# Kernel optimization log

Measured on AMD Instinct MI355X. Metric: run time of the kernel, lower is better.

The kernel has to match this reference:

```python
import jax, jax.numpy as jnp
import numpy as np

EPS = 1e-15  # 0.1 ** 15 in the original


def _mi_table(T):
    # Mutual information of a joint-probability table T [nx, ny]
    P_x = jnp.sum(T, axis=1)  # [nx]
    P_y = jnp.sum(T, axis=0)  # [ny]
    T_xy = P_x[:, None] * P_y[None, :]  # outer product [nx, ny]
    mi = jnp.sum(T * (jnp.log((T + EPS) / (T_xy + EPS)) / jnp.log(jnp.float32(2.0))))
    return mi


def setup_inputs() -> dict:
    key = jax.random.key(0)
    k1, k2 = jax.random.split(key)
    N_ins, N_att, K = 16384, 8192, 64
    Ur = jax.random.uniform(k1, (N_ins, K), dtype=jnp.float32)
    Uc = jax.random.uniform(k2, (N_att, K), dtype=jnp.float32)
    return {"Ur": Ur, "Uc": Uc, "nclu_row": K, "nclu_col": K}


def reference(Ur, Uc, nclu_row, nclu_col):
    # joint probability table  [N_ins, N_att]
    T = Ur @ Uc.T
    T = T / jnp.sum(T)

    v1 = jnp.argmax(Ur, axis=1)  # hard row-cluster ids  [N_ins]
    v2 = jnp.argmax(Uc, axis=1)  # hard col-cluster ids  [N_att]

    # Reduce_Table: segment-sum rows then columns (replaces looped mask+concat)
    T_r = jax.ops.segment_sum(T, v1, num_segments=nclu_row)          # [nclu_row, N_att]
    T_rr = jax.ops.segment_sum(T_r.T, v2, num_segments=nclu_col).T  # [nclu_row, nclu_col]

    mi_org = _mi_table(T)
    mi_red = _mi_table(T_rr)

    loss = jnp.log(1.0 + jnp.abs(1.0 - mi_red / mi_org))
    return loss
```

## Files before the change

### kernel.cpp

```cpp
#include <hip/hip_runtime.h>
#include <hip/hip_bf16.h>

#define N_INS 16384
#define N_ATT 8192
#define KDIM  64

typedef __attribute__((ext_vector_type(8))) short bf16x8;
typedef __attribute__((ext_vector_type(4))) float f32x4;

#define OFF_UCB    0
#define OFF_CPR    1048576
#define OFF_CPC    1064960
#define OFF_ASEG   1073152
#define OFF_BSEG   1089536
#define OFF_GACC   1105920
#define OFF_TK     1106688

#define NBLK_SEG   96
#define NBLK_U     96
#define NBLK_HEAVY 2048
#define NBLK_K2    (NBLK_SEG + NBLK_U + NBLK_HEAVY)

__device__ __forceinline__ unsigned short f2bf(float x) {
    unsigned u = __float_as_uint(x);
    u = (u + 0x7FFFu + ((u >> 16) & 1u)) >> 16;
    return (unsigned short)u;
}

__device__ __forceinline__ float wave_red(float v) {
#pragma unroll
    for (int o = 32; o > 0; o >>= 1) v += __shfl_down(v, o, 64);
    return v;
}

typedef __attribute__((address_space(3))) unsigned int as3_u32;
typedef const __attribute__((address_space(1))) unsigned int as1_u32;
__device__ __forceinline__ void stage16(void* l, const void* g) {
    __builtin_amdgcn_global_load_lds((as1_u32*)g, (as3_u32*)l, 16, 0, 0);
}

__global__ __launch_bounds__(256)
void k_prep(const float* __restrict__ Ur, const float* __restrict__ Uc,
            float* __restrict__ cpr, float* __restrict__ cpc,
            unsigned short* __restrict__ Ucb,
            float* __restrict__ Aseg, float* __restrict__ Bseg,
            double* __restrict__ Gacc, unsigned* __restrict__ tickets) {
    __shared__ float cs2[256];
    int blk = blockIdx.x, tid = threadIdx.x;
    if (blk < 128) {
        int gid = blk * 256 + tid;
        for (int c = gid; c < N_ATT * 8; c += 32768) {
            int t = c >> 7, o = c & 127;
            int q, m;
            if (o < 64) { q = o >> 4; m = o & 15; }
            else        { q = 4 + ((o - 64) >> 4); m = (o - 64) & 15; }
            int r = t * 16 + m;
            const float4* src = (const float4*)(Uc + (size_t)r * 64 + q * 8);
            float4 x0 = src[0], x1 = src[1];
            uint4 v;
            v.x = (unsigned)f2bf(x0.x) | ((unsigned)f2bf(x0.y) << 16);
            v.y = (unsigned)f2bf(x0.z) | ((unsigned)f2bf(x0.w) << 16);
            v.z = (unsigned)f2bf(x1.x) | ((unsigned)f2bf(x1.y) << 16);
            v.w = (unsigned)f2bf(x1.z) | ((unsigned)f2bf(x1.w) << 16);
            *(uint4*)((unsigned char*)Ucb + (size_t)c * 16) = v;
        }
        return;
    }
    if (blk == 224) {
        float4 z4 = {0.f, 0.f, 0.f, 0.f};
        for (int i = tid; i < 1024; i += 256) ((float4*)Aseg)[i] = z4;
        for (int i = tid; i < 1024; i += 256) ((float4*)Bseg)[i] = z4;
        if (tid < 96) Gacc[tid] = 0.0;
        if (tid < 64) { tickets[tid] = 0u; tickets[64 + tid] = 0u;
                        tickets[128 + tid] = 0u; tickets[192 + tid] = 0u; }
        if (tid < 16) tickets[256 + tid] = 0u;
        return;
    }
    bool isUr = blk < 192;
    int b = isUr ? (blk - 128) : (blk - 192);
    const float* base = (isUr ? Ur : Uc) + (size_t)b * 256 * KDIM;
    float* dst = (isUr ? cpr : cpc) + b * 64;
    int col = tid & 63, r0 = tid >> 6;
    float s = 0.f;
    for (int r = r0; r < 256; r += 4) s += base[r * KDIM + col];
    cs2[tid] = s;
    __syncthreads();
    if (tid < 64) dst[tid] = cs2[tid] + cs2[tid + 64] + cs2[tid + 128] + cs2[tid + 192];
}

__global__ __launch_bounds__(256)
void k_main(const float* __restrict__ Ur, const float* __restrict__ Uc,
            const unsigned char* __restrict__ Ucb,
            const float* __restrict__ cpr, const float* __restrict__ cpc,
            float* __restrict__ Aseg, float* __restrict__ Bseg,
            double* __restrict__ Gacc, unsigned* __restrict__ tickets,
            float* __restrict__ out) {
    __shared__ __align__(16) unsigned char smem[17408];
    __shared__ int flagS;
    int tid = threadIdx.x, blk = blockIdx.x;
    int wvi = tid >> 6, lane = tid & 63;

    if (blk < NBLK_SEG) {
        float* Part = (float*)smem;
        int*   bins = (int*)(smem + 16384);
        bool isUr = blk < 64;
        int b = isUr ? blk : (blk - 64);
        const float* M = isUr ? Ur : Uc;
        float* Seg = isUr ? Aseg : Bseg;
        int base_row = b * 256;
        for (int i = tid; i < 4096; i += 256) Part[i] = 0.f;
        __syncthreads();
        {
            const float* rp = M + (size_t)(base_row + tid) * KDIM;
            float best = -1e30f; int bidx = 0;
#pragma unroll
            for (int k = 0; k < 64; k += 4) {
                float4 v = *(const float4*)(rp + k);
                if (v.x > best) { best = v.x; bidx = k; }
                if (v.y > best) { best = v.y; bidx = k + 1; }
                if (v.z > best) { best = v.z; bidx = k + 2; }
                if (v.w > best) { best = v.w; bidx = k + 3; }
            }
            bins[tid] = bidx;
        }
        __syncthreads();
        {
            int r0 = wvi * 64;
            const float* Mb = M + (size_t)(base_row + r0) * 64 + lane;
#pragma unroll 4
            for (int r = 0; r < 64; ++r) {
                int bb = bins[r0 + r];
                float val = Mb[(size_t)r * 64];
                atomicAdd(&Part[bb * 64 + lane], val);
            }
        }
        __syncthreads();
        for (int i = tid; i < 4096; i += 256)
            atomicAdd(&Seg[i], Part[i]);
    } else if (blk < NBLK_SEG + NBLK_U) {
        float* wv = (float*)smem;
        bool isUr = blk < (NBLK_SEG + 64);
        int b = isUr ? (blk - NBLK_SEG) : (blk - NBLK_SEG - 64);
        const float* M = isUr ? Ur : Uc;
        int base_row = b * 256;
        if (tid < 64) {
            const float* cpw = isUr ? cpc : cpr;
            int nbw = isUr ? 32 : 64;
            float s = 0.f;
            for (int p = 0; p < nbw; ++p) s += cpw[p * 64 + tid];
            wv[tid] = s;
        }
        __syncthreads();
        const float* rp = M + (size_t)(base_row + tid) * KDIM;
        float u = 0.f;
#pragma unroll
        for (int k = 0; k < 64; k += 4) {
            float4 v = *(const float4*)(rp + k);
            u += v.x * wv[k] + v.y * wv[k + 1] + v.z * wv[k + 2] + v.w * wv[k + 3];
        }
        float pw = wave_red(u * __log2f(u));
        if (lane == 0)
            atomicAdd(&Gacc[(isUr ? 64 : 80) + (b & 15)], (double)pw);
    } else {
        unsigned char* bufs = smem;
        float* gshW = (float*)(smem + 16384);
        int hb = blk - NBLK_SEG - NBLK_U;
        int quad = lane >> 4, m = lane & 15;
        int rb = hb & 127, cc = hb >> 7;
        int row0 = rb * 128 + wvi * 32;
        bf16x8 a[2][2];
#pragma unroll
        for (int t = 0; t < 2; ++t) {
            int ridx = row0 + t * 16 + m;
            const float* rp = Ur + (size_t)ridx * 64 + quad * 8;
#pragma unroll
            for (int h = 0; h < 2; ++h) {
                const float* rph = rp + h * 32;
                float4 x0 = *(const float4*)rph;
                float4 x1 = *(const float4*)(rph + 4);
                bf16x8 f;
                f[0] = (short)f2bf(x0.x); f[1] = (short)f2bf(x0.y);
                f[2] = (short)f2bf(x0.z); f[3] = (short)f2bf(x0.w);
                f[4] = (short)f2bf(x1.x); f[5] = (short)f2bf(x1.y);
                f[6] = (short)f2bf(x1.z); f[7] = (short)f2bf(x1.w);
                a[t][h] = f;
            }
        }
        const unsigned char* gB = Ucb + (size_t)(cc * 32) * 2048;
        int soff = wvi * 2048 + lane * 16;
        stage16(bufs + soff, gB + soff);
        stage16(bufs + soff + 1024, gB + soff + 1024);
        int loff = lane * 16;
        float g = 0.f;
#pragma unroll 1
        for (int pg = 0; pg < 8; ++pg) {
            __syncthreads();
            if (pg < 7) {
                const unsigned char* gn = gB + (size_t)(pg + 1) * 8192;
                unsigned char* bn = bufs + (((pg + 1) & 1) << 13);
                stage16(bn + soff, gn + soff);
                stage16(bn + soff + 1024, gn + soff + 1024);
            }
            const unsigned char* bg = bufs + ((pg & 1) << 13);
#pragma unroll
            for (int p = 0; p < 2; ++p) {
                const unsigned char* bb = bg + p * 4096;
                bf16x8 c00 = *(const bf16x8*)(bb + loff);
                bf16x8 c01 = *(const bf16x8*)(bb + 1024 + loff);
                bf16x8 c10 = *(const bf16x8*)(bb + 2048 + loff);
                bf16x8 c11 = *(const bf16x8*)(bb + 3072 + loff);
                f32x4 acc00 = {0.f,0.f,0.f,0.f}, acc01 = {0.f,0.f,0.f,0.f};
                f32x4 acc10 = {0.f,0.f,0.f,0.f}, acc11 = {0.f,0.f,0.f,0.f};
                acc00 = __builtin_amdgcn_mfma_f32_16x16x32_bf16(a[0][0], c00, acc00, 0, 0, 0);
                acc00 = __builtin_amdgcn_mfma_f32_16x16x32_bf16(a[0][1], c01, acc00, 0, 0, 0);
                acc10 = __builtin_amdgcn_mfma_f32_16x16x32_bf16(a[1][0], c00, acc10, 0, 0, 0);
                acc10 = __builtin_amdgcn_mfma_f32_16x16x32_bf16(a[1][1], c01, acc10, 0, 0, 0);
                acc01 = __builtin_amdgcn_mfma_f32_16x16x32_bf16(a[0][0], c10, acc01, 0, 0, 0);
                acc01 = __builtin_amdgcn_mfma_f32_16x16x32_bf16(a[0][1], c11, acc01, 0, 0, 0);
                acc11 = __builtin_amdgcn_mfma_f32_16x16x32_bf16(a[1][0], c10, acc11, 0, 0, 0);
                acc11 = __builtin_amdgcn_mfma_f32_16x16x32_bf16(a[1][1], c11, acc11, 0, 0, 0);
#pragma unroll
                for (int e = 0; e < 4; ++e) {
                    float d0 = acc00[e]; g += d0 * __log2f(d0);
                    float d1 = acc01[e]; g += d1 * __log2f(d1);
                    float d2 = acc10[e]; g += d2 * __log2f(d2);
                    float d3 = acc11[e]; g += d3 * __log2f(d3);
                }
            }
        }
        float gw = wave_red(g);
        if (lane == 0) gshW[wvi] = gw;
        __syncthreads();
        if (tid == 0) {
            float gs = gshW[0] + gshW[1] + gshW[2] + gshW[3];
            atomicAdd(&Gacc[hb & 63], (double)gs);
        }
    }

    __builtin_amdgcn_s_waitcnt(0);
    __syncthreads();
    if (tid == 0) {
        flagS = 0;
        unsigned old = atomicAdd(&tickets[(blk & 15) << 4], 1u);
        if (old == (NBLK_K2 / 16) - 1) {
            unsigned old2 = atomicAdd(&tickets[256], 1u);
            flagS = (old2 == 15u);
        }
    }
    __syncthreads();
    if (!flagS) return;

    float*  Prx = (float*)smem;
    float*  Pry = (float*)(smem + 256);
    double* sc  = (double*)(smem + 512);
    double* red = (double*)(smem + 1024);
    if (tid < 64) {
        double sa = 0.0, sb = 0.0;
        for (int p = 0; p < 64; ++p) sa += (double)cpr[p * 64 + tid];
        for (int p = 0; p < 32; ++p) sb += (double)cpc[p * 64 + tid];
        red[tid] = sa * sb;
        Prx[tid] = 0.f; Pry[tid] = 0.f;
    }
    __syncthreads();
    if (tid == 0) {
        double s = 0.0;
        for (int k = 0; k < 64; ++k) s += red[k];
        sc[0] = s;
        double gg = 0.0;
        for (int k = 0; k < 64; ++k) gg += Gacc[k];
        sc[1] = gg;
    } else if (tid == 1) {
        double s = 0.0;
        for (int k = 64; k < 80; ++k) s += Gacc[k];
        sc[2] = s;
    } else if (tid == 2) {
        double s = 0.0;
        for (int k = 80; k < 96; ++k) s += Gacc[k];
        sc[3] = s;
    }
    __syncthreads();
    double S = sc[0];
    int p = tid >> 2, q0 = (tid & 3) * 16;
    float tloc[16];
    {
        float prow_sum = 0.f;
        for (int qi = 0; qi < 16; ++qi) {
            int q = q0 + qi;
            double s = 0.0;
            for (int k = 0; k < 64; ++k)
                s += (double)Aseg[p * 64 + k] * (double)Bseg[q * 64 + k];
            float t = (float)(s / S);
            tloc[qi] = t;
            prow_sum += t;
            atomicAdd(&Pry[q], t);
        }
        atomicAdd(&Prx[p], prow_sum);
    }
    __syncthreads();
    {
        const double EPSd = 1e-15;
        double part = 0.0;
        for (int qi = 0; qi < 16; ++qi) {
            double t = (double)tloc[qi];
            double txy = (double)Prx[p] * (double)Pry[q0 + qi];
            part += t * log((t + EPSd) / (txy + EPSd));
        }
        red[tid] = part;
    }
    __syncthreads();
    for (int s2 = 128; s2 > 0; s2 >>= 1) {
        if (tid < s2) red[tid] += red[tid + s2];
        __syncthreads();
    }
    if (tid == 0) {
        const double inv_ln2 = 1.4426950408889634;
        double mi_red = red[0] * inv_ln2;
        double G = sc[1], Uu = sc[2], Vv = sc[3];
        double log2S = log(S) * inv_ln2;
        double mi_org = G / S + log2S - (Uu + Vv) / S;
        double loss = log(1.0 + fabs(1.0 - mi_red / mi_org));
        out[0] = (float)loss;
    }
}

extern "C" void kernel_launch(void* const* d_in, const int* in_sizes, int n_in,
                              void* d_out, int out_size, void* d_ws, size_t ws_size,
                              hipStream_t stream) {
    const float* Ur = (const float*)d_in[0];
    const float* Uc = (const float*)d_in[1];
    float* out = (float*)d_out;
    char* ws = (char*)d_ws;
    unsigned short* Ucb = (unsigned short*)(ws + OFF_UCB);
    float* cpr   = (float*)(ws + OFF_CPR);
    float* cpc   = (float*)(ws + OFF_CPC);
    float* Aseg  = (float*)(ws + OFF_ASEG);
    float* Bseg  = (float*)(ws + OFF_BSEG);
    double* Gacc = (double*)(ws + OFF_GACC);
    unsigned* tickets = (unsigned*)(ws + OFF_TK);

    k_prep<<<225, 256, 0, stream>>>(Ur, Uc, cpr, cpc, Ucb, Aseg, Bseg, Gacc, tickets);
    k_main<<<NBLK_K2, 256, 0, stream>>>(Ur, Uc, (const unsigned char*)Ucb,
                                        cpr, cpc, Aseg, Bseg, Gacc, tickets, out);
}
```

Measured before the change: 161.7 us.

## Read Uc bf16 tiles directly from global and consolidate segment-sum blocks

The heavy MFMA blocks no longer stage Uc bf16 tiles into LDS with double-buffered global_load_lds plus block barriers. They now read the fragments straight from global memory, relying on cache, with the loop unrolled by two. The segment-sum phase uses 16 larger blocks that process 2048 or 1024 rows each. Each block splits the 64 bins into two passes, storing bins as bytes, which shrinks the shared footprint so more blocks fit per CU. The trade is repeated global and L2 traffic and more serial work in fewer seg blocks, in exchange for fewer barriers and fewer global atomics.

```diff
diff --git a/kernel.cpp b/kernel.cpp
--- a/kernel.cpp
+++ b/kernel.cpp
@@ -16,7 +16,7 @@
 #define OFF_GACC   1105920
 #define OFF_TK     1106688
 
-#define NBLK_SEG   96
+#define NBLK_SEG   16
 #define NBLK_U     96
 #define NBLK_HEAVY 2048
 #define NBLK_K2    (NBLK_SEG + NBLK_U + NBLK_HEAVY)
@@ -31,12 +31,6 @@
 #pragma unroll
     for (int o = 32; o > 0; o >>= 1) v += __shfl_down(v, o, 64);
     return v;
-}
-
-typedef __attribute__((address_space(3))) unsigned int as3_u32;
-typedef const __attribute__((address_space(1))) unsigned int as1_u32;
-__device__ __forceinline__ void stage16(void* l, const void* g) {
-    __builtin_amdgcn_global_load_lds((as1_u32*)g, (as3_u32*)l, 16, 0, 0);
 }
 
 __global__ __launch_bounds__(256)
@@ -95,23 +89,21 @@
             float* __restrict__ Aseg, float* __restrict__ Bseg,
             double* __restrict__ Gacc, unsigned* __restrict__ tickets,
             float* __restrict__ out) {
-    __shared__ __align__(16) unsigned char smem[17408];
+    __shared__ __align__(16) unsigned char smem[10240];
     __shared__ int flagS;
     int tid = threadIdx.x, blk = blockIdx.x;
     int wvi = tid >> 6, lane = tid & 63;
 
     if (blk < NBLK_SEG) {
         float* Part = (float*)smem;
-        int*   bins = (int*)(smem + 16384);
-        bool isUr = blk < 64;
-        int b = isUr ? blk : (blk - 64);
-        const float* M = isUr ? Ur : Uc;
+        unsigned char* bins8 = smem + 8192;
+        bool isUr = blk < 8;
+        int b = blk & 7;
+        int R = isUr ? 2048 : 1024;
+        const float* M = (isUr ? Ur : Uc) + (size_t)b * R * KDIM;
         float* Seg = isUr ? Aseg : Bseg;
-        int base_row = b * 256;
-        for (int i = tid; i < 4096; i += 256) Part[i] = 0.f;
-        __syncthreads();
-        {
-            const float* rp = M + (size_t)(base_row + tid) * KDIM;
+        for (int r = tid; r < R; r += 256) {
+            const float* rp = M + (size_t)r * KDIM;
             float best = -1e30f; int bidx = 0;
 #pragma unroll
             for (int k = 0; k < 64; k += 4) {
@@ -121,22 +113,28 @@
                 if (v.z > best) { best = v.z; bidx = k + 2; }
                 if (v.w > best) { best = v.w; bidx = k + 3; }
             }
-            bins[tid] = bidx;
+            bins8[r] = (unsigned char)bidx;
         }
         __syncthreads();
-        {
-            int r0 = wvi * 64;
-            const float* Mb = M + (size_t)(base_row + r0) * 64 + lane;
+        int cnt = R >> 2;
+        int r0 = wvi * cnt;
+        const float* Mb = M + (size_t)r0 * 64 + lane;
+        for (int half = 0; half < 2; ++half) {
+            for (int i = tid; i < 2048; i += 256) Part[i] = 0.f;
+            __syncthreads();
 #pragma unroll 4
-            for (int r = 0; r < 64; ++r) {
-                int bb = bins[r0 + r];
-                float val = Mb[(size_t)r * 64];
-                atomicAdd(&Part[bb * 64 + lane], val);
+            for (int r = 0; r < cnt; ++r) {
+                int bb = bins8[r0 + r];
+                if ((bb >> 5) == half) {
+                    float val = Mb[(size_t)r * 64];
+                    atomicAdd(&Part[(bb & 31) * 64 + lane], val);
+                }
             }
-        }
-        __syncthreads();
-        for (int i = tid; i < 4096; i += 256)
-            atomicAdd(&Seg[i], Part[i]);
+            __syncthreads();
+            for (int i = tid; i < 2048; i += 256)
+                atomicAdd(&Seg[(half << 11) + i], Part[i]);
+            __syncthreads();
+        }
     } else if (blk < NBLK_SEG + NBLK_U) {
         float* wv = (float*)smem;
         bool isUr = blk < (NBLK_SEG + 64);
@@ -162,8 +160,7 @@
         if (lane == 0)
             atomicAdd(&Gacc[(isUr ? 64 : 80) + (b & 15)], (double)pw);
     } else {
-        unsigned char* bufs = smem;
-        float* gshW = (float*)(smem + 16384);
+        float* gshW = (float*)smem;
         int hb = blk - NBLK_SEG - NBLK_U;
         int quad = lane >> 4, m = lane & 15;
         int rb = hb & 127, cc = hb >> 7;
@@ -187,21 +184,11 @@
             }
         }
         const unsigned char* gB = Ucb + (size_t)(cc * 32) * 2048;
-        int soff = wvi * 2048 + lane * 16;
-        stage16(bufs + soff, gB + soff);
-        stage16(bufs + soff + 1024, gB + soff + 1024);
         int loff = lane * 16;
         float g = 0.f;
-#pragma unroll 1
+#pragma unroll 2
         for (int pg = 0; pg < 8; ++pg) {
-            __syncthreads();
-            if (pg < 7) {
-                const unsigned char* gn = gB + (size_t)(pg + 1) * 8192;
-                unsigned char* bn = bufs + (((pg + 1) & 1) << 13);
-                stage16(bn + soff, gn + soff);
-                stage16(bn + soff + 1024, gn + soff + 1024);
-            }
-            const unsigned char* bg = bufs + ((pg & 1) << 13);
+            const unsigned char* bg = gB + (size_t)pg * 8192;
 #pragma unroll
             for (int p = 0; p < 2; ++p) {
                 const unsigned char* bb = bg + p * 4096;
```

Result: slower. 358.5 us (+121.7%).
